# Optimization experiments

Hardware: AMD Instinct MI355X
Metric: run time of the kernel (lower is better)

The kernel has to match this reference:

```python
import jax, jax.numpy as jnp
import numpy as np

NUM_FEATURES = 1_000_000
EMB_DIM = 16
NUM_FIELDS = 39
CIN_SIZES = (200, 200, 200)
DNN_SIZES = (400, 400)


def setup_inputs() -> dict:
    key = jax.random.key(0)
    ks = jax.random.split(key, 16)
    B = 2048
    inp = {}
    inp["feature_ids"] = jax.random.randint(ks[0], (B, NUM_FIELDS), 0, NUM_FEATURES)
    inp["feature_vals"] = jax.random.uniform(ks[1], (B, NUM_FIELDS), dtype=jnp.float32)
    # embeddings (xavier-normal-ish scale)
    inp["emb"] = jax.random.normal(ks[2], (NUM_FEATURES, EMB_DIM), jnp.float32) * 0.02
    inp["bias_emb"] = jax.random.normal(ks[3], (NUM_FEATURES, 1), jnp.float32) * 0.02
    # CIN conv1d (kernel size 1) weights: (out, in)
    field_nums = [NUM_FIELDS]
    for i, size in enumerate(CIN_SIZES):
        cin_in = field_nums[-1] * NUM_FIELDS
        inp[f"cin_W{i}"] = jax.random.normal(ks[4 + i], (size, cin_in), jnp.float32) / np.sqrt(cin_in)
        inp[f"cin_b{i}"] = jnp.zeros((size,), jnp.float32)
        field_nums.append(size // 2 if i != len(CIN_SIZES) - 1 else size)
    # DNN linears: (out, in)
    last = NUM_FIELDS * EMB_DIM
    for i, size in enumerate(DNN_SIZES):
        inp[f"dnn_W{i}"] = jax.random.normal(ks[8 + i], (size, last), jnp.float32) / np.sqrt(last)
        inp[f"dnn_b{i}"] = jnp.zeros((size,), jnp.float32)
        last = size
    hidden_size = sum(CIN_SIZES[:-1]) // 2 + CIN_SIZES[-1]  # 400
    fc_in = hidden_size + DNN_SIZES[-1]
    inp["fc_W"] = jax.random.normal(ks[12], (1, fc_in), jnp.float32) / np.sqrt(fc_in)
    inp["fc_b"] = jnp.zeros((1,), jnp.float32)
    return inp


def _forward(feature_ids, feature_vals, emb, bias_emb,
             cin_W0, cin_b0, cin_W1, cin_b1, cin_W2, cin_b2,
             dnn_W0, dnn_b0, dnn_W1, dnn_b1, fc_W, fc_b):
    B = feature_ids.shape[0]
    inputs = emb[feature_ids] * feature_vals[:, :, None]        # [B, F, D]
    input_biases = bias_emb[feature_ids][..., 0] * feature_vals  # [B, F]

    # CIN
    Ws = (cin_W0, cin_W1, cin_W2)
    bs = (cin_b0, cin_b1, cin_b2)
    h = inputs
    finals = []
    n_layers = len(CIN_SIZES)
    for i in range(n_layers):
        size = CIN_SIZES[i]
        x = jnp.einsum('bhd,bmd->bhmd', h, inputs)              # [B, H, F, D]
        x = x.reshape(B, -1, EMB_DIM)                           # [B, H*F, D]
        x = jnp.einsum('bcd,oc->bod', x, Ws[i]) + bs[i][None, :, None]  # 1x1 conv
        x = jax.nn.relu(x)
        if i != n_layers - 1:
            h, direct = x[:, : size // 2], x[:, size // 2:]
        else:
            direct = x
        finals.append(direct)
    cin_result = jnp.sum(jnp.concatenate(finals, axis=1), axis=-1)  # [B, hidden]

    # DNN
    d = inputs.reshape(B, -1)
    d = jax.nn.relu(d @ dnn_W0.T + dnn_b0)
    d = jax.nn.relu(d @ dnn_W1.T + dnn_b1)

    out = (jnp.concatenate((cin_result, d), axis=1) @ fc_W.T + fc_b)[:, 0]
    return out + jnp.sum(input_biases, axis=1)                  # [B]


def reference(feature_ids, feature_vals, emb, bias_emb,
              cin_W0, cin_b0, cin_W1, cin_b1, cin_W2, cin_b2,
              dnn_W0, dnn_b0, dnn_W1, dnn_b1, fc_W, fc_b):
    return _forward(feature_ids, feature_vals, emb, bias_emb,
                    cin_W0, cin_b0, cin_W1, cin_b1, cin_W2, cin_b2,
                    dnn_W0, dnn_b0, dnn_W1, dnn_b1, fc_W, fc_b)
```

## Files before the change

kernel.cpp:

```cpp
#include <hip/hip_runtime.h>

#define B 2048
#define NF 39
#define D 16

typedef __bf16 bf16x8 __attribute__((ext_vector_type(8)));
typedef float f32x4 __attribute__((ext_vector_type(4)));

__device__ __forceinline__ void lds_barrier() {
  asm volatile("s_waitcnt lgkmcnt(0)" ::: "memory");
  __builtin_amdgcn_s_barrier();
}

__device__ __forceinline__ void prep_cin_one(const float* __restrict__ W,
                                             __bf16* __restrict__ Wg,
                                             int Hreal, int idx) {
  int l = idx & 63;
  int mt = (idx >> 6) % 13;
  int c = idx / (13 * 64);
  int o = mt * 16 + (l & 15);
  int kb = c * 32 + ((l >> 4) << 3);
  int rowlen = Hreal * 39;
  bf16x8 v;
#pragma unroll
  for (int j = 0; j < 8; ++j) {
    int k = kb + j;
    int h = k / 40;
    int m = k - h * 40;
    float val = 0.f;
    if (o < 200 && h < Hreal && m < 39) val = W[(long)o * rowlen + h * 39 + m];
    v[j] = (__bf16)val;
  }
  *reinterpret_cast<bf16x8*>(Wg + (long)idx * 8) = v;
}

__device__ __forceinline__ void prep_dnn_one(const float* __restrict__ W,
                                             __bf16* __restrict__ Wd,
                                             int IN, int idx) {
  int l = idx & 63;
  int tt = (idx >> 6) % 25;
  int c = idx / (25 * 64);
  int o = tt * 16 + (l & 15);
  int kb = c * 32 + ((l >> 4) << 3);
  bf16x8 v;
#pragma unroll
  for (int j = 0; j < 8; ++j) {
    int k = kb + j;
    v[j] = (k < IN) ? (__bf16)W[(long)o * IN + k] : (__bf16)0.f;
  }
  *reinterpret_cast<bf16x8*>(Wd + (long)idx * 8) = v;
}

#define PREP_T0 (50 * 13 * 64)
#define PREP_T12 (126 * 13 * 64)
#define PREP_T3 (20 * 25 * 64)
#define PREP_T4 (13 * 25 * 64)
#define PREP_TOTAL (PREP_T0 + 2 * PREP_T12 + PREP_T3 + PREP_T4)
#define PREP_BLOCKS ((PREP_TOTAL + 255) / 256)

__global__ __launch_bounds__(256) void gather_prep(
    const int* __restrict__ fid, const float* __restrict__ fval,
    const float* __restrict__ emb, const float* __restrict__ bias_emb,
    float* __restrict__ inputs, float* __restrict__ biassum,
    const float* __restrict__ cW0, const float* __restrict__ cW1,
    const float* __restrict__ cW2, const float* __restrict__ dW0,
    const float* __restrict__ dW1, __bf16* __restrict__ Wg0,
    __bf16* __restrict__ Wg1, __bf16* __restrict__ Wg2,
    __bf16* __restrict__ Wd0, __bf16* __restrict__ Wd1) {
  int t = threadIdx.x;
  if (blockIdx.x < B) {
    int b = blockIdx.x;
    __shared__ int ids[NF];
    __shared__ float vals[NF];
    if (t < NF) { ids[t] = fid[b * NF + t]; vals[t] = fval[b * NF + t]; }
    __syncthreads();
    for (int i = t; i < NF * D; i += 256) {
      int f = i >> 4, d = i & 15;
      inputs[b * NF * D + i] = emb[(long)ids[f] * D + d] * vals[f];
    }
    if (t < 64) {
      float pb = (t < NF) ? bias_emb[ids[t]] * vals[t] : 0.f;
#pragma unroll
      for (int m = 32; m >= 1; m >>= 1) pb += __shfl_xor(pb, m);
      if (t == 0) biassum[b] = pb;
    }
    return;
  }
  int idx = (blockIdx.x - B) * 256 + t;
  if (idx < PREP_T0) { prep_cin_one(cW0, Wg0, 39, idx); return; }
  idx -= PREP_T0;
  if (idx < PREP_T12) { prep_cin_one(cW1, Wg1, 100, idx); return; }
  idx -= PREP_T12;
  if (idx < PREP_T12) { prep_cin_one(cW2, Wg2, 100, idx); return; }
  idx -= PREP_T12;
  if (idx < PREP_T3) { prep_dnn_one(dW0, Wd0, 624, idx); return; }
  idx -= PREP_T3;
  if (idx < PREP_T4) prep_dnn_one(dW1, Wd1, 400, idx);
}

__device__ __forceinline__ void form_x(const float* Hs, const float* Zs,
                                       __bf16* xbuf, int k0, int col) {
  int h = (int)((unsigned)k0 / 40u);
  int m0 = k0 - h * 40;
  float hv = Hs[h * 64 + col];
  const float4* zp = reinterpret_cast<const float4*>(Zs + col * 44 + m0);
  float4 za = zp[0], zb = zp[1];
  bf16x8 xv;
  xv[0] = (__bf16)(hv * za.x); xv[1] = (__bf16)(hv * za.y);
  xv[2] = (__bf16)(hv * za.z); xv[3] = (__bf16)(hv * za.w);
  xv[4] = (__bf16)(hv * zb.x); xv[5] = (__bf16)(hv * zb.y);
  xv[6] = (__bf16)(hv * zb.z); xv[7] = (__bf16)(hv * zb.w);
  int g = (k0 >> 3) & 7;
  *reinterpret_cast<bf16x8*>(
      reinterpret_cast<char*>(xbuf) + col * 128 + ((g * 16) ^ ((col & 7) << 4))) = xv;
}

template <int NW, int NST, int SPLIT>
__device__ __forceinline__ void cin_layer(
    float* Hs, const float* Zs, __bf16* Xs,
    const __bf16* __restrict__ Wg, const float* __restrict__ bias,
    float* __restrict__ cin_out, int col_offset, int bbase, int t) {
  constexpr int TLO = (13 * NW) >> 2;
  const int l = t & 63;
  const int q = l >> 4, dd = l & 15;

  f32x4 acc[13] = {};
  bf16x8 wf[8], wfn[8];
  const __bf16* wp = Wg + l * 8 + TLO * 512;
#pragma unroll
  for (int i = 0; i < 4; ++i)
#pragma unroll
    for (int hf = 0; hf < 2; ++hf)
      wf[i * 2 + hf] = *reinterpret_cast<const bf16x8*>(wp + hf * 6656 + i * 512);

  form_x(Hs, Zs, Xs, NW * 8, l);
  form_x(Hs, Zs, Xs, (NW + 4) * 8, l);
  lds_barrier();

  for (int s = 0; s < NST; ++s) {
    __bf16* xcur = Xs + (s & 1) * 4096;
    __bf16* xnxt = Xs + ((s + 1) & 1) * 4096;
    const bool more = (s + 1 < NST);
    if (more) {
      const __bf16* wq = wp + 13312;
#pragma unroll
      for (int i = 0; i < 4; ++i)
#pragma unroll
        for (int hf = 0; hf < 2; ++hf)
          wfn[i * 2 + hf] =
              *reinterpret_cast<const bf16x8*>(wq + hf * 6656 + i * 512);
    }
    bf16x8 bfr[4][2];
#pragma unroll
    for (int f = 0; f < 4; ++f)
#pragma unroll
      for (int hf = 0; hf < 2; ++hf) {
        int col = f * 16 + dd;
        int g = q + hf * 4;
        bfr[f][hf] = *reinterpret_cast<const bf16x8*>(
            reinterpret_cast<const char*>(xcur) + col * 128 +
            ((g * 16) ^ ((col & 7) << 4)));
      }
    if (more) {
      form_x(Hs, Zs, xnxt, (s + 1) * 64 + NW * 8, l);
      form_x(Hs, Zs, xnxt, (s + 1) * 64 + (NW + 4) * 8, l);
    }
    __builtin_amdgcn_s_setprio(1);
#pragma unroll
    for (int i = 0; i < 13; ++i) {
      const int p = 13 * NW + i;
      const int ti = (p >> 2) - TLO;
      const int f = p & 3;
      acc[i] = __builtin_amdgcn_mfma_f32_16x16x32_bf16(wf[ti * 2 + 0], bfr[f][0],
                                                       acc[i], 0, 0, 0);
      acc[i] = __builtin_amdgcn_mfma_f32_16x16x32_bf16(wf[ti * 2 + 1], bfr[f][1],
                                                       acc[i], 0, 0, 0);
    }
    __builtin_amdgcn_s_setprio(0);
    lds_barrier();
    if (more) {
#pragma unroll
      for (int i = 0; i < 8; ++i) wf[i] = wfn[i];
      wp += 13312;
    }
  }

#pragma unroll
  for (int i = 0; i < 13; ++i) {
    const int p = 13 * NW + i;
    const int tt = p >> 2, f = p & 3;
    const int b = bbase + f;
#pragma unroll
    for (int r = 0; r < 4; ++r) {
      int o = tt * 16 + q * 4 + r;
      if (o < 200) {
        float x = fmaxf(acc[i][r] + bias[o], 0.f);
        if (SPLIT && o < 100) {
          Hs[o * 64 + f * 16 + dd] = x;
        } else {
          x += __shfl_xor(x, 1);
          x += __shfl_xor(x, 2);
          x += __shfl_xor(x, 4);
          x += __shfl_xor(x, 8);
          if (dd == 0) cin_out[b * 400 + col_offset + o - (SPLIT ? 100 : 0)] = x;
        }
      }
    }
  }
  lds_barrier();
}

template <int NW>
__device__ __forceinline__ void cin_all(
    float* Hs, const float* Zs, __bf16* Xs, const __bf16* Wg0,
    const __bf16* Wg1, const __bf16* Wg2, const float* cb0, const float* cb1,
    const float* cb2, float* cinres, int bbase, int t) {
  cin_layer<NW, 25, 1>(Hs, Zs, Xs, Wg0, cb0, cinres, 0, bbase, t);
  cin_layer<NW, 63, 1>(Hs, Zs, Xs, Wg1, cb1, cinres, 100, bbase, t);
  cin_layer<NW, 63, 0>(Hs, Zs, Xs, Wg2, cb2, cinres, 200, bbase, t);
}

__global__ __launch_bounds__(256, 2) void cin_fused(
    const float* __restrict__ Zin, const __bf16* __restrict__ Wg0,
    const __bf16* __restrict__ Wg1, const __bf16* __restrict__ Wg2,
    const float* __restrict__ cb0, const float* __restrict__ cb1,
    const float* __restrict__ cb2, float* __restrict__ cinres) {
  __shared__ float Hs[101 * 64];
  __shared__ float Zs[64 * 44];
  __shared__ __bf16 Xs[2 * 64 * 64];
  const int t = threadIdx.x;
  const int bbase = blockIdx.x * 4;

  for (int i = t; i < 64 * 40; i += 256) {
    int col = i / 40, m = i - (i / 40) * 40;
    int b = bbase + (col >> 4), d = col & 15;
    Zs[col * 44 + m] = (m < NF) ? Zin[((long)b * NF + m) * 16 + d] : 0.f;
  }
  for (int i = t; i < 41 * 64; i += 256) {
    int h = i >> 6, col = i & 63;
    int b = bbase + (col >> 4), d = col & 15;
    Hs[i] = (h < NF) ? Zin[((long)b * NF + h) * 16 + d] : 0.f;
  }
  if (t < 64) Hs[100 * 64 + t] = 0.f;
  __syncthreads();

  const int w = t >> 6;
  if (w == 0) cin_all<0>(Hs, Zs, Xs, Wg0, Wg1, Wg2, cb0, cb1, cb2, cinres, bbase, t);
  else if (w == 1) cin_all<1>(Hs, Zs, Xs, Wg0, Wg1, Wg2, cb0, cb1, cb2, cinres, bbase, t);
  else if (w == 2) cin_all<2>(Hs, Zs, Xs, Wg0, Wg1, Wg2, cb0, cb1, cb2, cinres, bbase, t);
  else cin_all<3>(Hs, Zs, Xs, Wg0, Wg1, Wg2, cb0, cb1, cb2, cinres, bbase, t);
}

template <int IN>
__device__ __forceinline__ void dnn_stage_load(const float* __restrict__ x,
                                               int bg, int c, int t,
                                               float4& a, float4& b2) {
  int b = t >> 2, kb = t & 3;
  int k0 = c * 32 + kb * 8;
  if (k0 < IN) {
    const float4* p =
        reinterpret_cast<const float4*>(x + (long)(bg * 64 + b) * IN + k0);
    a = p[0];
    b2 = p[1];
  } else {
    a = make_float4(0.f, 0.f, 0.f, 0.f);
    b2 = make_float4(0.f, 0.f, 0.f, 0.f);
  }
}

__device__ __forceinline__ void dnn_stage_write(__bf16* Xs, int t, float4 a,
                                                float4 b2) {
  int b = t >> 2, kb = t & 3;
  bf16x8 v;
  v[0] = (__bf16)a.x;  v[1] = (__bf16)a.y;  v[2] = (__bf16)a.z;  v[3] = (__bf16)a.w;
  v[4] = (__bf16)b2.x; v[5] = (__bf16)b2.y; v[6] = (__bf16)b2.z; v[7] = (__bf16)b2.w;
  *reinterpret_cast<bf16x8*>(Xs + ((kb * 64 + b) << 3)) = v;
}

template <int IN, int NCH>
__global__ __launch_bounds__(256) void dnn_mfma2(
    const float* __restrict__ x, const __bf16* __restrict__ Wd,
    const float* __restrict__ bias, float* __restrict__ out) {
  __shared__ __bf16 Xs[2 * 2048];
  const int bg = blockIdx.x / 25;
  const int tile = blockIdx.x - bg * 25;
  const int t = threadIdx.x;
  const int w = t >> 6, l = t & 63;
  const int q = l >> 4, dd = l & 15;
  const __bf16* wl = Wd + l * 8;

  f32x4 acc = {};
  bf16x8 wf = *reinterpret_cast<const bf16x8*>(wl + (long)(tile * 64) * 8);

  float4 ra, rb;
  dnn_stage_load<IN>(x, bg, 0, t, ra, rb);
  dnn_stage_write(Xs, t, ra, rb);
  lds_barrier();

  for (int c = 0; c < NCH; ++c) {
    __bf16* cur = Xs + (c & 1) * 2048;
    __bf16* nxt = Xs + ((c + 1) & 1) * 2048;
    const bool more = (c + 1 < NCH);
    bf16x8 wfn;
    if (more) {
      dnn_stage_load<IN>(x, bg, c + 1, t, ra, rb);
      wfn = *reinterpret_cast<const bf16x8*>(
          wl + (long)(((c + 1) * 25 + tile) * 64) * 8);
    }
    bf16x8 bfr = *reinterpret_cast<const bf16x8*>(cur + ((q * 64 + w * 16 + dd) << 3));
    acc = __builtin_amdgcn_mfma_f32_16x16x32_bf16(wf, bfr, acc, 0, 0, 0);
    if (more) dnn_stage_write(nxt, t, ra, rb);
    lds_barrier();
    if (more) wf = wfn;
  }

  const int b = bg * 64 + w * 16 + dd;
#pragma unroll
  for (int r = 0; r < 4; ++r) {
    int o = tile * 16 + q * 4 + r;
    out[(long)b * 400 + o] = fmaxf(acc[r] + bias[o], 0.f);
  }
}

__global__ __launch_bounds__(256) void final_kernel(
    const float* __restrict__ cin, const float* __restrict__ d1,
    const float* __restrict__ fcW, const float* __restrict__ fcb,
    const float* __restrict__ biassum, float* __restrict__ out) {
  int b = blockIdx.x, t = threadIdx.x;
  float p = 0.f;
  for (int i = t; i < 800; i += 256) {
    float v = (i < 400) ? cin[b * 400 + i] : d1[b * 400 + (i - 400)];
    p += v * fcW[i];
  }
#pragma unroll
  for (int m = 32; m >= 1; m >>= 1) p += __shfl_xor(p, m);
  __shared__ float red[4];
  if ((t & 63) == 0) red[t >> 6] = p;
  __syncthreads();
  if (t == 0) out[b] = red[0] + red[1] + red[2] + red[3] + fcb[0] + biassum[b];
}

extern "C" void kernel_launch(void* const* d_in, const int* in_sizes, int n_in,
                              void* d_out, int out_size, void* d_ws,
                              size_t ws_size, hipStream_t stream) {
  (void)in_sizes; (void)n_in; (void)out_size; (void)ws_size;
  const int* fid = (const int*)d_in[0];
  const float* fval = (const float*)d_in[1];
  const float* emb = (const float*)d_in[2];
  const float* bias_emb = (const float*)d_in[3];
  const float* cW0 = (const float*)d_in[4];
  const float* cb0 = (const float*)d_in[5];
  const float* cW1 = (const float*)d_in[6];
  const float* cb1 = (const float*)d_in[7];
  const float* cW2 = (const float*)d_in[8];
  const float* cb2 = (const float*)d_in[9];
  const float* dW0 = (const float*)d_in[10];
  const float* db0 = (const float*)d_in[11];
  const float* dW1 = (const float*)d_in[12];
  const float* db1 = (const float*)d_in[13];
  const float* fcW = (const float*)d_in[14];
  const float* fcb = (const float*)d_in[15];
  float* out = (float*)d_out;

  float* ws = (float*)d_ws;
  float* inputs = ws;  ws += B * NF * D;
  float* biassum = ws; ws += B;
  float* cinres = ws;  ws += B * 400;
  float* dd0 = ws;     ws += B * 400;
  float* dd1 = ws;     ws += B * 400;
  __bf16* Wg0 = (__bf16*)ws; ws += (50 * 13 * 64 * 8) / 2;
  __bf16* Wg1 = (__bf16*)ws; ws += (126 * 13 * 64 * 8) / 2;
  __bf16* Wg2 = (__bf16*)ws; ws += (126 * 13 * 64 * 8) / 2;
  __bf16* Wd0 = (__bf16*)ws; ws += (20 * 25 * 64 * 8) / 2;
  __bf16* Wd1 = (__bf16*)ws; ws += (13 * 25 * 64 * 8) / 2;

  gather_prep<<<B + PREP_BLOCKS, 256, 0, stream>>>(
      fid, fval, emb, bias_emb, inputs, biassum,
      cW0, cW1, cW2, dW0, dW1, Wg0, Wg1, Wg2, Wd0, Wd1);

  cin_fused<<<B / 4, 256, 0, stream>>>(inputs, Wg0, Wg1, Wg2, cb0, cb1, cb2, cinres);

  dnn_mfma2<624, 20><<<800, 256, 0, stream>>>(inputs, Wd0, db0, dd0);
  dnn_mfma2<400, 13><<<800, 256, 0, stream>>>(dd0, Wd1, db1, dd1);

  final_kernel<<<B, 256, 0, stream>>>(cinres, dd1, fcW, fcb, biassum, out);
}
```

Measured before the change: 196.4 us.

## Split CIN kernel into producer waves forming X and consumer MFMA waves

The fused CIN kernel now runs 512 threads per block. Four producer waves build the bf16 outer-product tiles in LDS, and four consumer waves only load weights and issue MFMAs. Both sides step in lockstep through matching LDS barriers. The aim is to take the X-formation ALU and LDS writes off the MFMA waves' critical path so they overlap with matrix math. In exchange, doubling the wave count under launch_bounds(512,2) halves the register budget per wave, which risks spills in the consumer's large accumulator and weight-fragment set. It also relies on the barrier counts of the two roles staying in sync.

```diff
diff --git a/kernel.cpp b/kernel.cpp
--- a/kernel.cpp
+++ b/kernel.cpp
@@ -116,12 +116,11 @@
 }
 
 template <int NW, int NST, int SPLIT>
-__device__ __forceinline__ void cin_layer(
+__device__ __forceinline__ void cin_consumer(
     float* Hs, const float* Zs, __bf16* Xs,
     const __bf16* __restrict__ Wg, const float* __restrict__ bias,
-    float* __restrict__ cin_out, int col_offset, int bbase, int t) {
+    float* __restrict__ cin_out, int col_offset, int bbase, int l) {
   constexpr int TLO = (13 * NW) >> 2;
-  const int l = t & 63;
   const int q = l >> 4, dd = l & 15;
 
   f32x4 acc[13] = {};
@@ -133,13 +132,10 @@
     for (int hf = 0; hf < 2; ++hf)
       wf[i * 2 + hf] = *reinterpret_cast<const bf16x8*>(wp + hf * 6656 + i * 512);
 
-  form_x(Hs, Zs, Xs, NW * 8, l);
-  form_x(Hs, Zs, Xs, (NW + 4) * 8, l);
   lds_barrier();
 
   for (int s = 0; s < NST; ++s) {
     __bf16* xcur = Xs + (s & 1) * 4096;
-    __bf16* xnxt = Xs + ((s + 1) & 1) * 4096;
     const bool more = (s + 1 < NST);
     if (more) {
       const __bf16* wq = wp + 13312;
@@ -161,10 +157,6 @@
             reinterpret_cast<const char*>(xcur) + col * 128 +
             ((g * 16) ^ ((col & 7) << 4)));
       }
-    if (more) {
-      form_x(Hs, Zs, xnxt, (s + 1) * 64 + NW * 8, l);
-      form_x(Hs, Zs, xnxt, (s + 1) * 64 + (NW + 4) * 8, l);
-    }
     __builtin_amdgcn_s_setprio(1);
 #pragma unroll
     for (int i = 0; i < 13; ++i) {
@@ -210,17 +202,42 @@
   lds_barrier();
 }
 
+template <int PG, int NST>
+__device__ __forceinline__ void cin_producer(const float* Hs, const float* Zs,
+                                             __bf16* Xs, int l) {
+  form_x(Hs, Zs, Xs, PG * 8, l);
+  form_x(Hs, Zs, Xs, (PG + 4) * 8, l);
+  lds_barrier();
+  for (int s = 0; s < NST; ++s) {
+    if (s + 1 < NST) {
+      __bf16* xnxt = Xs + ((s + 1) & 1) * 4096;
+      form_x(Hs, Zs, xnxt, (s + 1) * 64 + PG * 8, l);
+      form_x(Hs, Zs, xnxt, (s + 1) * 64 + (PG + 4) * 8, l);
+    }
+    lds_barrier();
+  }
+  lds_barrier();
+}
+
 template <int NW>
-__device__ __forceinline__ void cin_all(
+__device__ __forceinline__ void cin_cons_all(
     float* Hs, const float* Zs, __bf16* Xs, const __bf16* Wg0,
     const __bf16* Wg1, const __bf16* Wg2, const float* cb0, const float* cb1,
-    const float* cb2, float* cinres, int bbase, int t) {
-  cin_layer<NW, 25, 1>(Hs, Zs, Xs, Wg0, cb0, cinres, 0, bbase, t);
-  cin_layer<NW, 63, 1>(Hs, Zs, Xs, Wg1, cb1, cinres, 100, bbase, t);
-  cin_layer<NW, 63, 0>(Hs, Zs, Xs, Wg2, cb2, cinres, 200, bbase, t);
-}
-
-__global__ __launch_bounds__(256, 2) void cin_fused(
+    const float* cb2, float* cinres, int bbase, int l) {
+  cin_consumer<NW, 25, 1>(Hs, Zs, Xs, Wg0, cb0, cinres, 0, bbase, l);
+  cin_consumer<NW, 63, 1>(Hs, Zs, Xs, Wg1, cb1, cinres, 100, bbase, l);
+  cin_consumer<NW, 63, 0>(Hs, Zs, Xs, Wg2, cb2, cinres, 200, bbase, l);
+}
+
+template <int PG>
+__device__ __forceinline__ void cin_prod_all(const float* Hs, const float* Zs,
+                                             __bf16* Xs, int l) {
+  cin_producer<PG, 25>(Hs, Zs, Xs, l);
+  cin_producer<PG, 63>(Hs, Zs, Xs, l);
+  cin_producer<PG, 63>(Hs, Zs, Xs, l);
+}
+
+__global__ __launch_bounds__(512, 2) void cin_pc(
     const float* __restrict__ Zin, const __bf16* __restrict__ Wg0,
     const __bf16* __restrict__ Wg1, const __bf16* __restrict__ Wg2,
     const float* __restrict__ cb0, const float* __restrict__ cb1,
@@ -231,12 +248,12 @@
   const int t = threadIdx.x;
   const int bbase = blockIdx.x * 4;
 
-  for (int i = t; i < 64 * 40; i += 256) {
+  for (int i = t; i < 64 * 40; i += 512) {
     int col = i / 40, m = i - (i / 40) * 40;
     int b = bbase + (col >> 4), d = col & 15;
     Zs[col * 44 + m] = (m < NF) ? Zin[((long)b * NF + m) * 16 + d] : 0.f;
   }
-  for (int i = t; i < 41 * 64; i += 256) {
+  for (int i = t; i < 41 * 64; i += 512) {
     int h = i >> 6, col = i & 63;
     int b = bbase + (col >> 4), d = col & 15;
     Hs[i] = (h < NF) ? Zin[((long)b * NF + h) * 16 + d] : 0.f;
@@ -245,10 +262,17 @@
   __syncthreads();
 
   const int w = t >> 6;
-  if (w == 0) cin_all<0>(Hs, Zs, Xs, Wg0, Wg1, Wg2, cb0, cb1, cb2, cinres, bbase, t);
-  else if (w == 1) cin_all<1>(Hs, Zs, Xs, Wg0, Wg1, Wg2, cb0, cb1, cb2, cinres, bbase, t);
-  else if (w == 2) cin_all<2>(Hs, Zs, Xs, Wg0, Wg1, Wg2, cb0, cb1, cb2, cinres, bbase, t);
-  else cin_all<3>(Hs, Zs, Xs, Wg0, Wg1, Wg2, cb0, cb1, cb2, cinres, bbase, t);
+  const int l = t & 63;
+  switch (w) {
+    case 0: cin_cons_all<0>(Hs, Zs, Xs, Wg0, Wg1, Wg2, cb0, cb1, cb2, cinres, bbase, l); break;
+    case 1: cin_cons_all<1>(Hs, Zs, Xs, Wg0, Wg1, Wg2, cb0, cb1, cb2, cinres, bbase, l); break;
+    case 2: cin_cons_all<2>(Hs, Zs, Xs, Wg0, Wg1, Wg2, cb0, cb1, cb2, cinres, bbase, l); break;
+    case 3: cin_cons_all<3>(Hs, Zs, Xs, Wg0, Wg1, Wg2, cb0, cb1, cb2, cinres, bbase, l); break;
+    case 4: cin_prod_all<0>(Hs, Zs, Xs, l); break;
+    case 5: cin_prod_all<1>(Hs, Zs, Xs, l); break;
+    case 6: cin_prod_all<2>(Hs, Zs, Xs, l); break;
+    default: cin_prod_all<3>(Hs, Zs, Xs, l); break;
+  }
 }
 
 template <int IN>
@@ -378,7 +402,7 @@
       fid, fval, emb, bias_emb, inputs, biassum,
       cW0, cW1, cW2, dW0, dW1, Wg0, Wg1, Wg2, Wd0, Wd1);
 
-  cin_fused<<<B / 4, 256, 0, stream>>>(inputs, Wg0, Wg1, Wg2, cb0, cb1, cb2, cinres);
+  cin_pc<<<B / 4, 512, 0, stream>>>(inputs, Wg0, Wg1, Wg2, cb0, cb1, cb2, cinres);
 
   dnn_mfma2<624, 20><<<800, 256, 0, stream>>>(inputs, Wd0, db0, dd0);
   dnn_mfma2<400, 13><<<800, 256, 0, stream>>>(dd0, Wd1, db1, dd1);
```

Result: slower. 237.5 us (+20.9%).
